# Kernel tuning notes

Measured on AMD Instinct MI355X. Metric: run time of the kernel, lower is better.

## Reference

```python
import jax, jax.numpy as jnp
import numpy as np

V, E, H, HC = 20000, 300, 512, 256
B, N, LE, NW, LW, NC, LC = 16, 64, 16, 8, 16, 64, 16


def _gru_dir(xg, W_hh, b_hh, reverse):
    # xg: [B, T, 3*Hc] precomputed input gates; returns final hidden [B, Hc]
    xs = jnp.swapaxes(xg, 0, 1)
    if reverse:
        xs = xs[::-1]
    h0 = jnp.zeros((xg.shape[0], W_hh.shape[1]), xg.dtype)

    def step(h, xt):
        hr, hz, hn = jnp.split(h @ W_hh.T + b_hh, 3, axis=-1)
        xr, xz, xn = jnp.split(xt, 3, axis=-1)
        r = jax.nn.sigmoid(xr + hr)
        z = jax.nn.sigmoid(xz + hz)
        n = jnp.tanh(xn + r * hn)
        return (1.0 - z) * n + z * h, None

    hT, _ = jax.lax.scan(step, h0, xs)
    return hT


def _bigru(x, Wif, Whf, bif, bhf, Wib, Whb, bib, bhb):
    # x: [B, T, D] -> concat(fwd final, bwd final) = [B, 2*Hc]  (matches torch h_n.permute(1,0,2).reshape)
    hf = _gru_dir(x @ Wif.T + bif, Whf, bhf, False)
    hb = _gru_dir(x @ Wib.T + bib, Whb, bhb, True)
    return jnp.concatenate([hf, hb], axis=-1)


def setup_inputs() -> dict:
    key = jax.random.key(0)
    ks = iter(jax.random.split(key, 64))
    f = lambda *s: jax.random.normal(next(ks), s, jnp.float32) * 0.05
    ri = lambda *s: jax.random.randint(next(ks), s, 0, V)
    return {
        "emb_table": f(V, E),
        "W_prj": f(H, E),
        "dn_Wif": f(3 * HC, H), "dn_Whf": f(3 * HC, HC), "dn_bif": f(3 * HC), "dn_bhf": f(3 * HC),
        "dn_Wib": f(3 * HC, H), "dn_Whb": f(3 * HC, HC), "dn_bib": f(3 * HC), "dn_bhb": f(3 * HC),
        "W_e": f(H, H), "W_l": f(H, H), "W_w": f(H, H),
        "Wg": f(H, H), "bg": f(H),
        "diff_Wif": f(3 * H, H), "diff_Whf": f(3 * H, H), "diff_bif": f(3 * H), "diff_bhf": f(3 * H),
        "diff_Wib": f(3 * H, H), "diff_Whb": f(3 * H, H), "diff_bib": f(3 * H), "diff_bhb": f(3 * H),
        "Wc": f(1, 2 * H), "bc": f(1),
        "Wa1": f(2 * H, 2 * H), "ba1": f(2 * H), "Wa2": f(1, 2 * H), "ba2": f(1),
        "local_adj": jnp.zeros((64, 64), jnp.float32),
        "obs": ri(B, 32),
        "local_graph": ri(64, 8),
        "entities": ri(B, N, LE),
        "locals_": ri(B, N, LE),
        "worlds": ri(B, N, NW, LW),
        "commands": ri(B, NC, LC),
    }


def reference(emb_table, W_prj,
              dn_Wif, dn_Whf, dn_bif, dn_bhf, dn_Wib, dn_Whb, dn_bib, dn_bhb,
              W_e, W_l, W_w, Wg, bg,
              diff_Wif, diff_Whf, diff_bif, diff_bhf, diff_Wib, diff_Whb, diff_bib, diff_bhb,
              Wc, bc, Wa1, ba1, Wa2, ba2,
              local_adj, obs, local_graph, entities, locals_, worlds, commands):
    dn = (dn_Wif, dn_Whf, dn_bif, dn_bhf, dn_Wib, dn_Whb, dn_bib, dn_bhb)
    emb = lambda ids: emb_table[ids] @ W_prj.T  # embedding lookup + no-bias projection to H

    b, n, le = entities.shape
    ent_h = _bigru(emb(entities).reshape(b * n, le, H), *dn).reshape(b, n, H)
    ll = locals_.shape[-1]
    loc_h = _bigru(emb(locals_).reshape(b * n, ll, H), *dn).reshape(b, n, H)
    nw, lw = worlds.shape[2], worlds.shape[3]
    w_h = _bigru(emb(worlds).reshape(b * n * nw, lw, H), *dn).reshape(b, n, nw, H)
    worlds_sum = (w_h @ W_w).sum(axis=2)  # [b, n, H]

    # torch.ones(H,H) + W_e  ==  broadcastable 1.0 + W_e
    graph_hidden = jax.nn.elu(ent_h @ (1.0 + W_e)) + jax.nn.elu(loc_h @ W_l) + worlds_sum
    graph_encoding = jax.nn.elu(jax.nn.elu(graph_hidden) @ Wg.T + bg)  # graph_prj (dropout=eval identity)

    # value network: 'diff' path
    diff_h = _bigru(graph_encoding, diff_Wif, diff_Whf, diff_bif, diff_bhf,
                    diff_Wib, diff_Whb, diff_bib, diff_bhb)  # [b, 2H]
    value = (diff_h @ Wc.T + bc).reshape(b, 1, 1)

    nc, lc = commands.shape[1], commands.shape[2]
    c_h = _bigru(emb(commands).reshape(b * nc, lc, H), *dn).reshape(b, nc, H)

    rep = jnp.concatenate([
        jnp.broadcast_to(c_h[:, None, :, :], (b, n, nc, H)),
        jnp.broadcast_to(graph_encoding[:, :, None, :], (b, n, nc, H)),
    ], axis=-1)  # [b, n, nc, 2H]
    s = jax.nn.elu(rep @ Wa1.T + ba1) @ Wa2.T + ba2  # att_cmd (dropout p=0)
    scores = s[..., 0].mean(axis=1)  # mean over entities -> [b, nc]

    mask = commands.sum(axis=2) > 0
    probs = jax.nn.softmax(jnp.where(mask, scores, -1e9), axis=1)
    index = jnp.argmax(probs, axis=1).reshape(1, b, 1)  # deterministic stand-in for multinomial(1)
    return scores, index, value
```

## Files before the change

kernel.cpp:

```cpp
#include <hip/hip_runtime.h>
#include <stdint.h>

#define DEVFN __device__ __forceinline__

typedef __attribute__((ext_vector_type(4))) float fx4;
typedef __attribute__((ext_vector_type(8))) short sx8;
typedef __bf16 bf16x8 __attribute__((ext_vector_type(8)));

DEVFN float eluf(float x){ return x>0.f ? x : __expf(x)-1.f; }
DEVFN float sigm(float x){ return 1.f/(1.f+__expf(-x)); }
DEVFN float tanhf_(float x){ float cx=fminf(10.f,fmaxf(-10.f,x)); float e=__expf(-2.f*cx); return (1.f-e)/(1.f+e); }

DEVFN fx4 MFMA(sx8 a, sx8 b, fx4 c){
  return __builtin_amdgcn_mfma_f32_16x16x32_bf16(
      __builtin_bit_cast(bf16x8,a), __builtin_bit_cast(bf16x8,b), c, 0,0,0);
}
DEVFN void splitf(float x, short& hi, short& lo){
  __bf16 h = (__bf16)x; hi = __builtin_bit_cast(short, h);
  __bf16 l = (__bf16)(x - (float)h); lo = __builtin_bit_cast(short, l);
}

struct TT { const float* src; float* dst; int srows, scols, drows; };
struct TTs { TT t[4]; };
__global__ void k_prep_t(TTs ts){
  TT tk = ts.t[blockIdx.y];
  size_t tot = (size_t)tk.drows * tk.srows;
  for (size_t i = (size_t)blockIdx.x*256 + threadIdx.x; i < tot; i += (size_t)gridDim.x*256){
    int c = (int)(i / tk.srows), r = (int)(i % tk.srows);
    tk.dst[i] = (c < tk.scols) ? tk.src[(size_t)r*tk.scols + c] : 0.f;
  }
}
struct PL { const float* src; __bf16* hi; __bf16* lo; size_t n; };
struct PLs { PL t[2]; };
__global__ void k_prep_planes(PLs ts){
  PL tk = ts.t[blockIdx.y];
  for (size_t i = (size_t)blockIdx.x*256 + threadIdx.x; i < tk.n; i += (size_t)gridDim.x*256){
    float x = tk.src[i];
    __bf16 h = (__bf16)x;
    tk.hi[i] = h; tk.lo[i] = (__bf16)(x - (float)h);
  }
}
struct BC { const float* src; __bf16* dst; size_t n; };
struct BCs { BC t[2]; };
__global__ void k_prep_b16(BCs ts){
  BC tk = ts.t[blockIdx.y];
  for (size_t i = (size_t)blockIdx.x*256 + threadIdx.x; i < tk.n; i += (size_t)gridDim.x*256)
    tk.dst[i] = (__bf16)tk.src[i];
}

template<int EPI, int OBF>
__global__ __launch_bounds__(256) void gemm_k(
    const float* __restrict__ A, const float* __restrict__ B,
    const float* __restrict__ bias, void* __restrict__ out,
    int M, int N, int Kpad, int Kreal, int lda, int ldb)
{
  int bm = blockIdx.x*64, bn = blockIdx.y*64;
  int tid = threadIdx.x, l = tid&63, w = tid>>6;
  int wm = (w>>1)*32, wn = (w&1)*32;
  int lr = l&15, lk = l>>4;
  fx4 acc[2][2] = {};
  for (int k0 = 0; k0 < Kpad; k0 += 32) {
    sx8 ahi[2], alo[2], bhi[2], blo[2];
    bool full = (k0 + 32 <= Kreal);
    #pragma unroll
    for (int i=0;i<2;i++){
      int row = bm + wm + i*16 + lr; row = row < M ? row : M-1;
      int col = bn + wn + i*16 + lr;
      const float* ap = A + (size_t)row*lda + k0 + lk*8;
      const float* bp = B + (size_t)col*ldb + k0 + lk*8;
      float av[8], bv[8];
      if (full){
        *(fx4*)av = *(const fx4*)ap; *(fx4*)(av+4) = *(const fx4*)(ap+4);
        *(fx4*)bv = *(const fx4*)bp; *(fx4*)(bv+4) = *(const fx4*)(bp+4);
      } else {
        #pragma unroll
        for (int j=0;j<8;j++){
          int k = k0 + lk*8 + j;
          av[j] = (k < Kreal) ? ap[j] : 0.f;
          bv[j] = (k < Kreal) ? bp[j] : 0.f;
        }
      }
      #pragma unroll
      for (int j=0;j<8;j++){
        short h,lo2; splitf(av[j], h, lo2); ahi[i][j]=h; alo[i][j]=lo2;
        splitf(bv[j], h, lo2); bhi[i][j]=h; blo[i][j]=lo2;
      }
    }
    #pragma unroll
    for (int i=0;i<2;i++)
      #pragma unroll
      for (int j=0;j<2;j++){
        acc[i][j] = MFMA(alo[i], bhi[j], acc[i][j]);
        acc[i][j] = MFMA(ahi[i], blo[j], acc[i][j]);
        acc[i][j] = MFMA(ahi[i], bhi[j], acc[i][j]);
      }
  }
  #pragma unroll
  for (int i=0;i<2;i++)
    #pragma unroll
    for (int j=0;j<2;j++)
      #pragma unroll
      for (int q=0;q<4;q++){
        int m = bm + wm + i*16 + lk*4 + q;
        int n = bn + wn + j*16 + lr;
        if (m < M){
          float v = acc[i][j][q];
          if (EPI>=1) v += bias[n];
          if (EPI==2) v = eluf(v);
          if (OBF) ((__bf16*)out)[(size_t)m*N + n] = (__bf16)v;
          else     ((float*)out)[(size_t)m*N + n] = v;
        }
      }
}

__global__ __launch_bounds__(512,2) void dn_gru(
  const float* __restrict__ T,
  const __bf16* __restrict__ Whi, const __bf16* __restrict__ Wlo,
  const float* __restrict__ bh,
  const int* __restrict__ ents, const int* __restrict__ locs,
  const int* __restrict__ wrl, const int* __restrict__ cmd,
  float* __restrict__ seqh, int dir)
{
  __shared__ __align__(16) __bf16 hhi[64*256];
  __shared__ __align__(16) __bf16 hlo[64*256];
  __shared__ int toks[64];
  int wg = blockIdx.x;
  int cb = wg*64;
  int tid = threadIdx.x, l = tid&63, wn = tid>>6;
  int lr = l&15, lk = l>>4;
  float bR[2], bZ[2], bN[2];
  #pragma unroll
  for (int jb=0;jb<2;jb++){
    int j = wn*32 + jb*16 + lr;
    bR[jb]=bh[j]; bZ[jb]=bh[256+j]; bN[jb]=bh[512+j];
  }
  for (int i=tid;i<64*256;i+=512){ hhi[i]=(__bf16)0.f; hlo[i]=(__bf16)0.f; }
  for (int s=0;s<16;s++){
    __syncthreads();
    if (tid<64){
      int c = cb+tid; const int* tp;
      if (c<1024) tp = ents + c*16;
      else if (c<2048) tp = locs + (c-1024)*16;
      else if (c<10240) tp = wrl + (c-2048)*16;
      else tp = cmd + (c-10240)*16;
      toks[tid] = tp[dir? 15-s : s];
    }
    __syncthreads();
    fx4 acc[4][6] = {};
    for (int kk=0;kk<8;kk++){
      sx8 ah[4], al[4];
      #pragma unroll
      for (int mt=0;mt<4;mt++){
        int row = mt*16 + lr;
        int c = (kk*4+lk) ^ (row&31);
        ah[mt] = *(const sx8*)&hhi[row*256 + c*8];
        al[mt] = *(const sx8*)&hlo[row*256 + c*8];
      }
      #pragma unroll
      for (int jb=0;jb<2;jb++)
        #pragma unroll
        for (int role=0;role<3;role++){
          int col = role*256 + wn*32 + jb*16 + lr;
          sx8 bh_ = *(const sx8*)(Whi + (size_t)col*256 + kk*32 + lk*8);
          sx8 bl_ = *(const sx8*)(Wlo + (size_t)col*256 + kk*32 + lk*8);
          #pragma unroll
          for (int mt=0;mt<4;mt++){
            fx4 a = acc[mt][jb*3+role];
            a = MFMA(al[mt], bh_, a);
            a = MFMA(ah[mt], bl_, a);
            a = MFMA(ah[mt], bh_, a);
            acc[mt][jb*3+role] = a;
          }
        }
    }
    float hnew[4][4][2];
    #pragma unroll
    for (int mt=0;mt<4;mt++){
      #pragma unroll
      for (int q=0;q<4;q++){
        int m = mt*16 + lk*4 + q;
        const float* trow = T + (size_t)toks[m]*768;
        #pragma unroll
        for (int jb=0;jb<2;jb++){
          int j = wn*32 + jb*16 + lr;
          float hr = acc[mt][jb*3+0][q] + bR[jb];
          float hz = acc[mt][jb*3+1][q] + bZ[jb];
          float hn = acc[mt][jb*3+2][q] + bN[jb];
          float xr = trow[j], xz = trow[256+j], xn = trow[512+j];
          int cc = ((j>>3) ^ (m&31));
          int hidx = m*256 + cc*8 + (j&7);
          float ho = (float)hhi[hidx] + (float)hlo[hidx];
          float r = sigm(xr+hr), z = sigm(xz+hz);
          float n = tanhf_(xn + r*hn);
          hnew[mt][q][jb] = (1.f-z)*n + z*ho;
        }
      }
    }
    if (s < 15){
      __syncthreads();
      #pragma unroll
      for (int mt=0;mt<4;mt++)
        #pragma unroll
        for (int q=0;q<4;q++)
          #pragma unroll
          for (int jb=0;jb<2;jb++){
            int m = mt*16 + lk*4 + q;
            int j = wn*32 + jb*16 + lr;
            int cc = ((j>>3) ^ (m&31));
            int hidx = m*256 + cc*8 + (j&7);
            float v = hnew[mt][q][jb];
            __bf16 h = (__bf16)v;
            hhi[hidx] = h; hlo[hidx] = (__bf16)(v - (float)h);
          }
    } else {
      #pragma unroll
      for (int mt=0;mt<4;mt++)
        #pragma unroll
        for (int q=0;q<4;q++)
          #pragma unroll
          for (int jb=0;jb<2;jb++){
            int m = mt*16 + lk*4 + q;
            int j = wn*32 + jb*16 + lr;
            seqh[(size_t)(cb+m)*512 + dir*256 + j] = hnew[mt][q][jb];
          }
    }
  }
}

__global__ void k_wsum(const float* __restrict__ seqh, float* __restrict__ ws){
  int r = blockIdx.x;
  for (int c = threadIdx.x; c < 512; c += 256){
    float a = 0.f;
    #pragma unroll
    for (int w8=0; w8<8; w8++) a += seqh[((size_t)2048 + r*8 + w8)*512 + c];
    ws[(size_t)r*512 + c] = a;
  }
}
__global__ void k_rowsum(const float* __restrict__ seqh, float* __restrict__ rs){
  int r = blockIdx.x, l = threadIdx.x;
  float a = 0.f;
  for (int c=l;c<512;c+=64) a += seqh[(size_t)r*512+c];
  #pragma unroll
  for (int o=32;o>0;o>>=1) a += __shfl_down(a,o);
  if (l==0) rs[r]=a;
}
__global__ void k_combine(const float* __restrict__ E1, const float* __restrict__ E2,
                          const float* __restrict__ E3, const float* __restrict__ rs,
                          float* __restrict__ y){
  size_t i = (size_t)blockIdx.x*256 + threadIdx.x;
  int r = (int)(i >> 9);
  float g = eluf(E1[i] + rs[r]) + eluf(E2[i]) + E3[i];
  y[i] = eluf(g);
}

__global__ __launch_bounds__(256) void diff_step(
  const float* __restrict__ hsrc, float* __restrict__ hdst,
  const __bf16* __restrict__ Whf, const __bf16* __restrict__ Whb,
  const float* __restrict__ bhf, const float* __restrict__ bhb,
  const __bf16* __restrict__ Xf, const __bf16* __restrict__ Xb, int t)
{
  int wg = blockIdx.x;
  int dir = wg>>3, seg = wg&7;
  const __bf16* W = dir? Whb: Whf;
  const float* bh = dir? bhb: bhf;
  const __bf16* X = dir? Xb: Xf;
  int tt = dir? 63-t : t;
  int tid = threadIdx.x, l = tid&63, w = tid>>6;
  int lr=l&15, lk=l>>4;
  int jbase = seg*64 + w*16;
  fx4 acc[3] = {};
  const float* hrow = hsrc + (size_t)dir*16*512;
  for (int kk=0;kk<16;kk++){
    const float* ap = hrow + (size_t)lr*512 + kk*32 + lk*8;
    float av[8];
    *(fx4*)av = *(const fx4*)ap; *(fx4*)(av+4) = *(const fx4*)(ap+4);
    sx8 ah, al;
    #pragma unroll
    for (int j=0;j<8;j++){ short h,lo; splitf(av[j],h,lo); ah[j]=h; al[j]=lo; }
    #pragma unroll
    for (int role=0;role<3;role++){
      int col = role*512 + jbase + lr;
      sx8 b = *(const sx8*)(W + (size_t)col*512 + kk*32 + lk*8);
      acc[role] = MFMA(al, b, acc[role]);
      acc[role] = MFMA(ah, b, acc[role]);
    }
  }
  #pragma unroll
  for (int q=0;q<4;q++){
    int m = lk*4+q;
    int j = jbase + lr;
    float hr = acc[0][q] + bh[j];
    float hz = acc[1][q] + bh[512+j];
    float hn = acc[2][q] + bh[1024+j];
    const __bf16* xrow = X + ((size_t)m*64 + tt)*1536;
    float xr = (float)xrow[j], xz = (float)xrow[512+j], xn = (float)xrow[1024+j];
    float ho = hrow[(size_t)m*512 + j];
    float r = sigm(xr+hr), z = sigm(xz+hz);
    float n = tanhf_(xn + r*hn);
    hdst[((size_t)dir*16 + m)*512 + j] = (1.f-z)*n + z*ho;
  }
}

__global__ __launch_bounds__(256) void k_score(
  const float* __restrict__ Amat, const float* __restrict__ Gmat,
  const float* __restrict__ Wa2, const float* __restrict__ ba2, float* __restrict__ sc)
{
  __shared__ float red[4];
  int p = blockIdx.x, b = p>>6, tid = threadIdx.x;
  float av[4], wv[4];
  #pragma unroll
  for (int k=0;k<4;k++){ av[k] = Amat[(size_t)p*1024 + tid + k*256]; wv[k] = Wa2[tid + k*256]; }
  float acc = 0.f;
  for (int n=0;n<64;n++){
    const float* g = Gmat + ((size_t)b*64+n)*1024;
    #pragma unroll
    for (int k=0;k<4;k++) acc += wv[k]*eluf(av[k] + g[tid + k*256]);
  }
  #pragma unroll
  for (int o=32;o>0;o>>=1) acc += __shfl_down(acc,o);
  if ((tid&63)==0) red[tid>>6] = acc;
  __syncthreads();
  if (tid==0) sc[p] = (red[0]+red[1]+red[2]+red[3])*(1.f/64.f) + ba2[0];
}

__global__ void k_final(const float* __restrict__ sc, const int* __restrict__ cmds,
                        const float* __restrict__ hfin, const float* __restrict__ Wc,
                        const float* __restrict__ bc, float* __restrict__ out)
{
  int b = blockIdx.x, l = threadIdx.x;
  out[b*64+l] = sc[b*64+l];
  int ssum = 0;
  const int* cr = cmds + (b*64+l)*16;
  #pragma unroll
  for (int k=0;k<16;k++) ssum += cr[k];
  float v = ssum>0 ? sc[b*64+l] : -1e9f;
  int idx = l;
  #pragma unroll
  for (int o=32;o>0;o>>=1){
    float ov = __shfl_down(v,o); int oi = __shfl_down(idx,o);
    if (ov > v || (ov==v && oi<idx)) { v=ov; idx=oi; }
  }
  if (l==0) out[1024 + b] = (float)idx;
  float a = 0.f;
  for (int j=l;j<512;j+=64) a += hfin[(size_t)b*512+j] * Wc[j];
  for (int j=l;j<512;j+=64) a += hfin[(size_t)(16+b)*512+j] * Wc[512+j];
  #pragma unroll
  for (int o=32;o>0;o>>=1) a += __shfl_down(a,o);
  if (l==0) out[1040 + b] = a + bc[0];
}

static inline void launch_gemm(hipStream_t st, const float* A, const float* B,
                               const float* bias, void* out, int M, int N,
                               int Kpad, int Kreal, int lda, int ldb, int epi, int obf)
{
  dim3 g((M+63)/64, N/64), blk(256);
  if      (epi==0 && obf==0) gemm_k<0,0><<<g,blk,0,st>>>(A,B,bias,out,M,N,Kpad,Kreal,lda,ldb);
  else if (epi==1 && obf==0) gemm_k<1,0><<<g,blk,0,st>>>(A,B,bias,out,M,N,Kpad,Kreal,lda,ldb);
  else if (epi==2 && obf==0) gemm_k<2,0><<<g,blk,0,st>>>(A,B,bias,out,M,N,Kpad,Kreal,lda,ldb);
  else                       gemm_k<1,1><<<g,blk,0,st>>>(A,B,bias,out,M,N,Kpad,Kreal,lda,ldb);
}

extern "C" void kernel_launch(void* const* d_in, const int* in_sizes, int n_in,
                              void* d_out, int out_size, void* d_ws, size_t ws_size,
                              hipStream_t stream) {
  (void)in_sizes; (void)n_in; (void)out_size; (void)ws_size;
  const float* emb   = (const float*)d_in[0];
  const float* W_prj = (const float*)d_in[1];
  const float* dnWif = (const float*)d_in[2];
  const float* dnWhf = (const float*)d_in[3];
  const float* dnbif = (const float*)d_in[4];
  const float* dnbhf = (const float*)d_in[5];
  const float* dnWib = (const float*)d_in[6];
  const float* dnWhb = (const float*)d_in[7];
  const float* dnbib = (const float*)d_in[8];
  const float* dnbhb = (const float*)d_in[9];
  const float* W_e   = (const float*)d_in[10];
  const float* W_l   = (const float*)d_in[11];
  const float* W_w   = (const float*)d_in[12];
  const float* Wg    = (const float*)d_in[13];
  const float* bg    = (const float*)d_in[14];
  const float* dWif  = (const float*)d_in[15];
  const float* dWhf  = (const float*)d_in[16];
  const float* dbif  = (const float*)d_in[17];
  const float* dbhf  = (const float*)d_in[18];
  const float* dWib  = (const float*)d_in[19];
  const float* dWhb  = (const float*)d_in[20];
  const float* dbib  = (const float*)d_in[21];
  const float* dbhb  = (const float*)d_in[22];
  const float* Wc    = (const float*)d_in[23];
  const float* bc    = (const float*)d_in[24];
  const float* Wa1   = (const float*)d_in[25];
  const float* ba1   = (const float*)d_in[26];
  const float* Wa2   = (const float*)d_in[27];
  const float* ba2   = (const float*)d_in[28];
  const int* ents = (const int*)d_in[32];
  const int* locs = (const int*)d_in[33];
  const int* wrl  = (const int*)d_in[34];
  const int* cmds = (const int*)d_in[35];

  char* ws = (char*)d_ws;
  size_t off = 0;
#define WSP(name, type, count) type* name = (type*)(ws + off); off += (((size_t)(count))*sizeof(type) + 255) & ~(size_t)255;
  WSP(pT,     float, 20000*768);
  WSP(pWprjT, float, 320*512);
  WSP(pCf,    float, 768*320);
  WSP(pCb,    float, 768*320);
  WSP(pWhFhi, __bf16, 768*256);
  WSP(pWhFlo, __bf16, 768*256);
  WSP(pWhBhi, __bf16, 768*256);
  WSP(pWhBlo, __bf16, 768*256);
  WSP(pWeT,   float, 512*512);
  WSP(pWlT,   float, 512*512);
  WSP(pWwT,   float, 512*512);
  WSP(pdWhF,  __bf16, 1536*512);
  WSP(pdWhB,  __bf16, 1536*512);
  WSP(pSeqh,  float, 11264*512);
  WSP(pWsum,  float, 1024*512);
  WSP(pRs,    float, 1024);
  WSP(pE1,    float, 1024*512);
  WSP(pE2,    float, 1024*512);
  WSP(pE3,    float, 1024*512);
  WSP(pY,     float, 1024*512);
  WSP(pGe,    float, 1024*512);
  WSP(pXf,    __bf16, 1024*1536);
  WSP(pXb,    __bf16, 1024*1536);
  WSP(pHA,    float, 32*512);
  WSP(pHB,    float, 32*512);
  WSP(pAmat,  float, 1024*1024);
  WSP(pGmat,  float, 1024*1024);
  WSP(pScf,   float, 1024);
#undef WSP

  TTs tt;
  tt.t[0] = { W_prj, pWprjT, 512, 300, 320 };
  tt.t[1] = { W_e,   pWeT,   512, 512, 512 };
  tt.t[2] = { W_l,   pWlT,   512, 512, 512 };
  tt.t[3] = { W_w,   pWwT,   512, 512, 512 };
  k_prep_t<<<dim3(256,4), 256, 0, stream>>>(tt);
  PLs pl;
  pl.t[0] = { dnWhf, pWhFhi, pWhFlo, (size_t)768*256 };
  pl.t[1] = { dnWhb, pWhBhi, pWhBlo, (size_t)768*256 };
  k_prep_planes<<<dim3(256,2), 256, 0, stream>>>(pl);
  BCs bcs;
  bcs.t[0] = { dWhf, pdWhF, (size_t)1536*512 };
  bcs.t[1] = { dWhb, pdWhB, (size_t)1536*512 };
  k_prep_b16<<<dim3(512,2), 256, 0, stream>>>(bcs);

  launch_gemm(stream, dnWif, pWprjT, nullptr, pCf, 768, 320, 512, 512, 512, 512, 0, 0);
  launch_gemm(stream, dnWib, pWprjT, nullptr, pCb, 768, 320, 512, 512, 512, 512, 0, 0);
  launch_gemm(stream, emb, pCf, dnbif, pT, 20000, 768, 320, 300, 300, 320, 1, 0);
  dn_gru<<<176, 512, 0, stream>>>(pT, pWhFhi, pWhFlo, dnbhf, ents, locs, wrl, cmds, pSeqh, 0);
  launch_gemm(stream, emb, pCb, dnbib, pT, 20000, 768, 320, 300, 300, 320, 1, 0);
  dn_gru<<<176, 512, 0, stream>>>(pT, pWhBhi, pWhBlo, dnbhb, ents, locs, wrl, cmds, pSeqh, 1);
  k_wsum<<<1024, 256, 0, stream>>>(pSeqh, pWsum);
  k_rowsum<<<1024, 64, 0, stream>>>(pSeqh, pRs);
  launch_gemm(stream, pSeqh,                   pWeT, nullptr, pE1, 1024, 512, 512, 512, 512, 512, 0, 0);
  launch_gemm(stream, pSeqh + (size_t)1024*512,pWlT, nullptr, pE2, 1024, 512, 512, 512, 512, 512, 0, 0);
  launch_gemm(stream, pWsum,                   pWwT, nullptr, pE3, 1024, 512, 512, 512, 512, 512, 0, 0);
  k_combine<<<2048, 256, 0, stream>>>(pE1, pE2, pE3, pRs, pY);
  launch_gemm(stream, pY, Wg, bg, pGe, 1024, 512, 512, 512, 512, 512, 2, 0);
  launch_gemm(stream, pGe, dWif, dbif, pXf, 1024, 1536, 512, 512, 512, 512, 1, 1);
  launch_gemm(stream, pGe, dWib, dbib, pXb, 1024, 1536, 512, 512, 512, 512, 1, 1);
  launch_gemm(stream, pSeqh + (size_t)10240*512, Wa1, nullptr, pAmat, 1024, 1024, 512, 512, 512, 1024, 0, 0);
  launch_gemm(stream, pGe, Wa1 + 512, ba1, pGmat, 1024, 1024, 512, 512, 512, 1024, 1, 0);
  k_score<<<1024, 256, 0, stream>>>(pAmat, pGmat, Wa2, ba2, pScf);
  hipMemsetAsync(pHA, 0, 32*512*sizeof(float), stream);
  float* ha = pHA; float* hb = pHB;
  for (int t=0; t<64; ++t){
    diff_step<<<16, 256, 0, stream>>>(ha, hb, pdWhF, pdWhB, dbhf, dbhb, pXf, pXb, t);
    float* tmp = ha; ha = hb; hb = tmp;
  }
  k_final<<<16, 64, 0, stream>>>(pScf, cmds, ha, Wc, bc, (float*)d_out);
}
```

Measured before the change: 3.473 ms.

## Fuse diff GRU timesteps into a persistent kernel with grid barrier; halve dn_gru tiles

Replaces 64 per-timestep diff_step launches with one persistent kernel. Its 16 workgroups step through time and synchronise through a global atomic counter barrier, which removes per-step launch overhead. The dn_gru kernel now processes 32 sequences per workgroup instead of 64, doubling the grid to 352 blocks so more CUs are busy, and it uses nontemporal loads and stores for the gate inputs and outputs. The spin barrier relies on all 16 blocks being co-resident, and the final h is still read from pHA, which holds the correct buffer after an even number of swaps.

```diff
diff --git a/kernel.cpp b/kernel.cpp
--- a/kernel.cpp
+++ b/kernel.cpp
@@ -121,11 +121,11 @@
   const int* __restrict__ wrl, const int* __restrict__ cmd,
   float* __restrict__ seqh, int dir)
 {
-  __shared__ __align__(16) __bf16 hhi[64*256];
-  __shared__ __align__(16) __bf16 hlo[64*256];
-  __shared__ int toks[64];
+  __shared__ __align__(16) __bf16 hhi[32*256];
+  __shared__ __align__(16) __bf16 hlo[32*256];
+  __shared__ int toks[32];
   int wg = blockIdx.x;
-  int cb = wg*64;
+  int cb = wg*32;
   int tid = threadIdx.x, l = tid&63, wn = tid>>6;
   int lr = l&15, lk = l>>4;
   float bR[2], bZ[2], bN[2];
@@ -134,10 +134,10 @@
     int j = wn*32 + jb*16 + lr;
     bR[jb]=bh[j]; bZ[jb]=bh[256+j]; bN[jb]=bh[512+j];
   }
-  for (int i=tid;i<64*256;i+=512){ hhi[i]=(__bf16)0.f; hlo[i]=(__bf16)0.f; }
+  for (int i=tid;i<32*256;i+=512){ hhi[i]=(__bf16)0.f; hlo[i]=(__bf16)0.f; }
   for (int s=0;s<16;s++){
     __syncthreads();
-    if (tid<64){
+    if (tid<32){
       int c = cb+tid; const int* tp;
       if (c<1024) tp = ents + c*16;
       else if (c<2048) tp = locs + (c-1024)*16;
@@ -146,11 +146,11 @@
       toks[tid] = tp[dir? 15-s : s];
     }
     __syncthreads();
-    fx4 acc[4][6] = {};
+    fx4 acc[2][6] = {};
     for (int kk=0;kk<8;kk++){
-      sx8 ah[4], al[4];
-      #pragma unroll
-      for (int mt=0;mt<4;mt++){
+      sx8 ah[2], al[2];
+      #pragma unroll
+      for (int mt=0;mt<2;mt++){
         int row = mt*16 + lr;
         int c = (kk*4+lk) ^ (row&31);
         ah[mt] = *(const sx8*)&hhi[row*256 + c*8];
@@ -164,7 +164,7 @@
           sx8 bh_ = *(const sx8*)(Whi + (size_t)col*256 + kk*32 + lk*8);
           sx8 bl_ = *(const sx8*)(Wlo + (size_t)col*256 + kk*32 + lk*8);
           #pragma unroll
-          for (int mt=0;mt<4;mt++){
+          for (int mt=0;mt<2;mt++){
             fx4 a = acc[mt][jb*3+role];
             a = MFMA(al[mt], bh_, a);
             a = MFMA(ah[mt], bl_, a);
@@ -173,9 +173,9 @@
           }
         }
     }
-    float hnew[4][4][2];
-    #pragma unroll
-    for (int mt=0;mt<4;mt++){
+    float hnew[2][4][2];
+    #pragma unroll
+    for (int mt=0;mt<2;mt++){
       #pragma unroll
       for (int q=0;q<4;q++){
         int m = mt*16 + lk*4 + q;
@@ -186,7 +186,9 @@
           float hr = acc[mt][jb*3+0][q] + bR[jb];
           float hz = acc[mt][jb*3+1][q] + bZ[jb];
           float hn = acc[mt][jb*3+2][q] + bN[jb];
-          float xr = trow[j], xz = trow[256+j], xn = trow[512+j];
+          float xr = __builtin_nontemporal_load(trow + j);
+          float xz = __builtin_nontemporal_load(trow + 256 + j);
+          float xn = __builtin_nontemporal_load(trow + 512 + j);
           int cc = ((j>>3) ^ (m&31));
           int hidx = m*256 + cc*8 + (j&7);
           float ho = (float)hhi[hidx] + (float)hlo[hidx];
@@ -199,7 +201,7 @@
     if (s < 15){
       __syncthreads();
       #pragma unroll
-      for (int mt=0;mt<4;mt++)
+      for (int mt=0;mt<2;mt++)
         #pragma unroll
         for (int q=0;q<4;q++)
           #pragma unroll
@@ -214,14 +216,14 @@
           }
     } else {
       #pragma unroll
-      for (int mt=0;mt<4;mt++)
+      for (int mt=0;mt<2;mt++)
         #pragma unroll
         for (int q=0;q<4;q++)
           #pragma unroll
           for (int jb=0;jb<2;jb++){
             int m = mt*16 + lk*4 + q;
             int j = wn*32 + jb*16 + lr;
-            seqh[(size_t)(cb+m)*512 + dir*256 + j] = hnew[mt][q][jb];
+            __builtin_nontemporal_store(hnew[mt][q][jb], &seqh[(size_t)(cb+m)*512 + dir*256 + j]);
           }
     }
   }
@@ -253,51 +255,67 @@
   y[i] = eluf(g);
 }
 
-__global__ __launch_bounds__(256) void diff_step(
-  const float* __restrict__ hsrc, float* __restrict__ hdst,
+__global__ __launch_bounds__(256) void diff_all(
+  float* __restrict__ hA, float* __restrict__ hB,
   const __bf16* __restrict__ Whf, const __bf16* __restrict__ Whb,
   const float* __restrict__ bhf, const float* __restrict__ bhb,
-  const __bf16* __restrict__ Xf, const __bf16* __restrict__ Xb, int t)
+  const __bf16* __restrict__ Xf, const __bf16* __restrict__ Xb,
+  unsigned* __restrict__ bar)
 {
   int wg = blockIdx.x;
   int dir = wg>>3, seg = wg&7;
   const __bf16* W = dir? Whb: Whf;
   const float* bh = dir? bhb: bhf;
   const __bf16* X = dir? Xb: Xf;
-  int tt = dir? 63-t : t;
   int tid = threadIdx.x, l = tid&63, w = tid>>6;
   int lr=l&15, lk=l>>4;
   int jbase = seg*64 + w*16;
-  fx4 acc[3] = {};
-  const float* hrow = hsrc + (size_t)dir*16*512;
-  for (int kk=0;kk<16;kk++){
-    const float* ap = hrow + (size_t)lr*512 + kk*32 + lk*8;
-    float av[8];
-    *(fx4*)av = *(const fx4*)ap; *(fx4*)(av+4) = *(const fx4*)(ap+4);
-    sx8 ah, al;
-    #pragma unroll
-    for (int j=0;j<8;j++){ short h,lo; splitf(av[j],h,lo); ah[j]=h; al[j]=lo; }
-    #pragma unroll
-    for (int role=0;role<3;role++){
-      int col = role*512 + jbase + lr;
-      sx8 b = *(const sx8*)(W + (size_t)col*512 + kk*32 + lk*8);
-      acc[role] = MFMA(al, b, acc[role]);
-      acc[role] = MFMA(ah, b, acc[role]);
-    }
-  }
-  #pragma unroll
-  for (int q=0;q<4;q++){
-    int m = lk*4+q;
-    int j = jbase + lr;
-    float hr = acc[0][q] + bh[j];
-    float hz = acc[1][q] + bh[512+j];
-    float hn = acc[2][q] + bh[1024+j];
-    const __bf16* xrow = X + ((size_t)m*64 + tt)*1536;
-    float xr = (float)xrow[j], xz = (float)xrow[512+j], xn = (float)xrow[1024+j];
-    float ho = hrow[(size_t)m*512 + j];
-    float r = sigm(xr+hr), z = sigm(xz+hz);
-    float n = tanhf_(xn + r*hn);
-    hdst[((size_t)dir*16 + m)*512 + j] = (1.f-z)*n + z*ho;
+  int j = jbase + lr;
+  float bRv = bh[j], bZv = bh[512+j], bNv = bh[1024+j];
+  float* hsrc = hA; float* hdst = hB;
+  for (int t=0; t<64; ++t){
+    int tt = dir? 63-t : t;
+    fx4 acc[3] = {};
+    const float* hrow = hsrc + (size_t)dir*16*512;
+    for (int kk=0;kk<16;kk++){
+      const float* ap = hrow + (size_t)lr*512 + kk*32 + lk*8;
+      float av[8];
+      *(fx4*)av = *(const fx4*)ap; *(fx4*)(av+4) = *(const fx4*)(ap+4);
+      sx8 ah, al;
+      #pragma unroll
+      for (int jj=0;jj<8;jj++){ short h,lo; splitf(av[jj],h,lo); ah[jj]=h; al[jj]=lo; }
+      #pragma unroll
+      for (int role=0;role<3;role++){
+        int col = role*512 + jbase + lr;
+        sx8 b = *(const sx8*)(W + (size_t)col*512 + kk*32 + lk*8);
+        acc[role] = MFMA(al, b, acc[role]);
+        acc[role] = MFMA(ah, b, acc[role]);
+      }
+    }
+    #pragma unroll
+    for (int q=0;q<4;q++){
+      int m = lk*4+q;
+      float hr = acc[0][q] + bRv;
+      float hz = acc[1][q] + bZv;
+      float hn = acc[2][q] + bNv;
+      const __bf16* xrow = X + ((size_t)m*64 + tt)*1536;
+      float xr = (float)xrow[j], xz = (float)xrow[512+j], xn = (float)xrow[1024+j];
+      float ho = hrow[(size_t)m*512 + j];
+      float r = sigm(xr+hr), z = sigm(xz+hz);
+      float n = tanhf_(xn + r*hn);
+      hdst[((size_t)dir*16 + m)*512 + j] = (1.f-z)*n + z*ho;
+    }
+    __threadfence();
+    __syncthreads();
+    if (tid==0){
+      atomicAdd(bar, 1u);
+      unsigned target = 16u*(unsigned)(t+1);
+      while (__hip_atomic_load(bar, __ATOMIC_RELAXED, __HIP_MEMORY_SCOPE_AGENT) < target)
+        __builtin_amdgcn_s_sleep(2);
+    }
+    __syncthreads();
+    __threadfence();
+    float* tmp = hsrc; hsrc = hdst; hdst = tmp;
   }
 }
 
@@ -429,6 +447,7 @@
   WSP(pAmat,  float, 1024*1024);
   WSP(pGmat,  float, 1024*1024);
   WSP(pScf,   float, 1024);
+  WSP(pBar,   unsigned, 64);
 #undef WSP
 
   TTs tt;
@@ -449,9 +468,9 @@
   launch_gemm(stream, dnWif, pWprjT, nullptr, pCf, 768, 320, 512, 512, 512, 512, 0, 0);
   launch_gemm(stream, dnWib, pWprjT, nullptr, pCb, 768, 320, 512, 512, 512, 512, 0, 0);
   launch_gemm(stream, emb, pCf, dnbif, pT, 20000, 768, 320, 300, 300, 320, 1, 0);
-  dn_gru<<<176, 512, 0, stream>>>(pT, pWhFhi, pWhFlo, dnbhf, ents, locs, wrl, cmds, pSeqh, 0);
+  dn_gru<<<352, 512, 0, stream>>>(pT, pWhFhi, pWhFlo, dnbhf, ents, locs, wrl, cmds, pSeqh, 0);
   launch_gemm(stream, emb, pCb, dnbib, pT, 20000, 768, 320, 300, 300, 320, 1, 0);
-  dn_gru<<<176, 512, 0, stream>>>(pT, pWhBhi, pWhBlo, dnbhb, ents, locs, wrl, cmds, pSeqh, 1);
+  dn_gru<<<352, 512, 0, stream>>>(pT, pWhBhi, pWhBlo, dnbhb, ents, locs, wrl, cmds, pSeqh, 1);
   k_wsum<<<1024, 256, 0, stream>>>(pSeqh, pWsum);
   k_rowsum<<<1024, 64, 0, stream>>>(pSeqh, pRs);
   launch_gemm(stream, pSeqh,                   pWeT, nullptr, pE1, 1024, 512, 512, 512, 512, 512, 0, 0);
@@ -465,10 +484,7 @@
   launch_gemm(stream, pGe, Wa1 + 512, ba1, pGmat, 1024, 1024, 512, 512, 512, 1024, 1, 0);
   k_score<<<1024, 256, 0, stream>>>(pAmat, pGmat, Wa2, ba2, pScf);
   hipMemsetAsync(pHA, 0, 32*512*sizeof(float), stream);
-  float* ha = pHA; float* hb = pHB;
-  for (int t=0; t<64; ++t){
-    diff_step<<<16, 256, 0, stream>>>(ha, hb, pdWhF, pdWhB, dbhf, dbhb, pXf, pXb, t);
-    float* tmp = ha; ha = hb; hb = tmp;
-  }
-  k_final<<<16, 64, 0, stream>>>(pScf, cmds, ha, Wc, bc, (float*)d_out);
-}
+  hipMemsetAsync(pBar, 0, 64*sizeof(unsigned), stream);
+  diff_all<<<16, 256, 0, stream>>>(pHA, pHB, pdWhF, pdWhB, dbhf, dbhb, pXf, pXb, pBar);
+  k_final<<<16, 64, 0, stream>>>(pScf, cmds, pHA, Wc, bc, (float*)d_out);
+}
```

Measured after the change: 4.519 ms. 30.1% more time.

## Split persistent GRU kernel into per-timestep launches with global hidden state

Applied to the files above, without the earlier changes.

Replaces the persistent dn_gru kernel (176 blocks, each holding the hidden state of 64 sequences in LDS across all 16 steps) with a per-timestep dn_step kernel launched on a 176x4 grid. The hidden state moves to ping-pong hi/lo bf16 buffers in global memory, and token indices are precomputed by a new k_toks kernel. The aim is more parallelism: four times as many blocks split the gate columns, so the GPU's CUs are better filled. In exchange it adds 32 kernel launches and global-memory round trips for the hidden state each step. Several scratch buffers now alias the pT region to save workspace.

```diff
diff --git a/kernel.cpp b/kernel.cpp
--- a/kernel.cpp
+++ b/kernel.cpp
@@ -46,6 +46,21 @@
   BC tk = ts.t[blockIdx.y];
   for (size_t i = (size_t)blockIdx.x*256 + threadIdx.x; i < tk.n; i += (size_t)gridDim.x*256)
     tk.dst[i] = (__bf16)tk.src[i];
+}
+__global__ void k_toks(const int* __restrict__ ents, const int* __restrict__ locs,
+                       const int* __restrict__ wrl, const int* __restrict__ cmd,
+                       int* __restrict__ toks){
+  int idx = blockIdx.x*256 + threadIdx.x;
+  if (idx >= 2*16*11264) return;
+  int dir = idx / (16*11264);
+  int rem = idx % (16*11264);
+  int s = rem / 11264, c = rem % 11264;
+  const int* tp;
+  if (c<1024) tp = ents + c*16;
+  else if (c<2048) tp = locs + (c-1024)*16;
+  else if (c<10240) tp = wrl + (c-2048)*16;
+  else tp = cmd + (c-10240)*16;
+  toks[idx] = tp[dir ? 15-s : s];
 }
 
 template<int EPI, int OBF>
@@ -113,116 +128,73 @@
       }
 }
 
-__global__ __launch_bounds__(512,2) void dn_gru(
-  const float* __restrict__ T,
+__global__ __launch_bounds__(256) void dn_step(
+  const __bf16* __restrict__ Hshi, const __bf16* __restrict__ Hslo,
+  __bf16* __restrict__ Hdhi, __bf16* __restrict__ Hdlo,
   const __bf16* __restrict__ Whi, const __bf16* __restrict__ Wlo,
-  const float* __restrict__ bh,
-  const int* __restrict__ ents, const int* __restrict__ locs,
-  const int* __restrict__ wrl, const int* __restrict__ cmd,
-  float* __restrict__ seqh, int dir)
-{
-  __shared__ __align__(16) __bf16 hhi[64*256];
-  __shared__ __align__(16) __bf16 hlo[64*256];
-  __shared__ int toks[64];
-  int wg = blockIdx.x;
-  int cb = wg*64;
-  int tid = threadIdx.x, l = tid&63, wn = tid>>6;
+  const float* __restrict__ bias, const float* __restrict__ T,
+  const int* __restrict__ toks,
+  float* __restrict__ seqh, int s, int dir)
+{
+  int bm = blockIdx.x*64;
+  int bj = blockIdx.y*64;
+  int tid = threadIdx.x, l = tid&63, w = tid>>6;
+  int wm = (w>>1)*32, wn = (w&1)*32;
   int lr = l&15, lk = l>>4;
-  float bR[2], bZ[2], bN[2];
-  #pragma unroll
-  for (int jb=0;jb<2;jb++){
-    int j = wn*32 + jb*16 + lr;
-    bR[jb]=bh[j]; bZ[jb]=bh[256+j]; bN[jb]=bh[512+j];
-  }
-  for (int i=tid;i<64*256;i+=512){ hhi[i]=(__bf16)0.f; hlo[i]=(__bf16)0.f; }
-  for (int s=0;s<16;s++){
-    __syncthreads();
-    if (tid<64){
-      int c = cb+tid; const int* tp;
-      if (c<1024) tp = ents + c*16;
-      else if (c<2048) tp = locs + (c-1024)*16;
-      else if (c<10240) tp = wrl + (c-2048)*16;
-      else tp = cmd + (c-10240)*16;
-      toks[tid] = tp[dir? 15-s : s];
-    }
-    __syncthreads();
-    fx4 acc[4][6] = {};
+  fx4 acc[2][2][3] = {};
+  if (s > 0){
     for (int kk=0;kk<8;kk++){
-      sx8 ah[4], al[4];
-      #pragma unroll
-      for (int mt=0;mt<4;mt++){
-        int row = mt*16 + lr;
-        int c = (kk*4+lk) ^ (row&31);
-        ah[mt] = *(const sx8*)&hhi[row*256 + c*8];
-        al[mt] = *(const sx8*)&hlo[row*256 + c*8];
-      }
-      #pragma unroll
-      for (int jb=0;jb<2;jb++)
+      sx8 ah[2], al[2];
+      #pragma unroll
+      for (int i=0;i<2;i++){
+        int m = bm + wm + i*16 + lr;
+        ah[i] = *(const sx8*)(Hshi + (size_t)m*256 + kk*32 + lk*8);
+        al[i] = *(const sx8*)(Hslo + (size_t)m*256 + kk*32 + lk*8);
+      }
+      #pragma unroll
+      for (int jt=0;jt<2;jt++){
         #pragma unroll
         for (int role=0;role<3;role++){
-          int col = role*256 + wn*32 + jb*16 + lr;
-          sx8 bh_ = *(const sx8*)(Whi + (size_t)col*256 + kk*32 + lk*8);
-          sx8 bl_ = *(const sx8*)(Wlo + (size_t)col*256 + kk*32 + lk*8);
+          int col = role*256 + bj + wn + jt*16 + lr;
+          sx8 bhf = *(const sx8*)(Whi + (size_t)col*256 + kk*32 + lk*8);
+          sx8 blf = *(const sx8*)(Wlo + (size_t)col*256 + kk*32 + lk*8);
           #pragma unroll
-          for (int mt=0;mt<4;mt++){
-            fx4 a = acc[mt][jb*3+role];
-            a = MFMA(al[mt], bh_, a);
-            a = MFMA(ah[mt], bl_, a);
-            a = MFMA(ah[mt], bh_, a);
-            acc[mt][jb*3+role] = a;
+          for (int i=0;i<2;i++){
+            fx4 a = acc[i][jt][role];
+            a = MFMA(al[i], bhf, a);
+            a = MFMA(ah[i], blf, a);
+            a = MFMA(ah[i], bhf, a);
+            acc[i][jt][role] = a;
           }
         }
+      }
     }
-    float hnew[4][4][2];
-    #pragma unroll
-    for (int mt=0;mt<4;mt++){
-      #pragma unroll
-      for (int q=0;q<4;q++){
-        int m = mt*16 + lk*4 + q;
-        const float* trow = T + (size_t)toks[m]*768;
-        #pragma unroll
-        for (int jb=0;jb<2;jb++){
-          int j = wn*32 + jb*16 + lr;
-          float hr = acc[mt][jb*3+0][q] + bR[jb];
-          float hz = acc[mt][jb*3+1][q] + bZ[jb];
-          float hn = acc[mt][jb*3+2][q] + bN[jb];
-          float xr = trow[j], xz = trow[256+j], xn = trow[512+j];
-          int cc = ((j>>3) ^ (m&31));
-          int hidx = m*256 + cc*8 + (j&7);
-          float ho = (float)hhi[hidx] + (float)hlo[hidx];
-          float r = sigm(xr+hr), z = sigm(xz+hz);
-          float n = tanhf_(xn + r*hn);
-          hnew[mt][q][jb] = (1.f-z)*n + z*ho;
-        }
-      }
-    }
-    if (s < 15){
-      __syncthreads();
-      #pragma unroll
-      for (int mt=0;mt<4;mt++)
-        #pragma unroll
-        for (int q=0;q<4;q++)
-          #pragma unroll
-          for (int jb=0;jb<2;jb++){
-            int m = mt*16 + lk*4 + q;
-            int j = wn*32 + jb*16 + lr;
-            int cc = ((j>>3) ^ (m&31));
-            int hidx = m*256 + cc*8 + (j&7);
-            float v = hnew[mt][q][jb];
-            __bf16 h = (__bf16)v;
-            hhi[hidx] = h; hlo[hidx] = (__bf16)(v - (float)h);
-          }
-    } else {
-      #pragma unroll
-      for (int mt=0;mt<4;mt++)
-        #pragma unroll
-        for (int q=0;q<4;q++)
-          #pragma unroll
-          for (int jb=0;jb<2;jb++){
-            int m = mt*16 + lk*4 + q;
-            int j = wn*32 + jb*16 + lr;
-            seqh[(size_t)(cb+m)*512 + dir*256 + j] = hnew[mt][q][jb];
-          }
+  }
+  const int* tks = toks + s*11264;
+  #pragma unroll
+  for (int i=0;i<2;i++){
+    #pragma unroll
+    for (int q=0;q<4;q++){
+      int m = bm + wm + i*16 + lk*4 + q;
+      int tok = tks[m];
+      const float* trow = T + (size_t)tok*768;
+      #pragma unroll
+      for (int jt=0;jt<2;jt++){
+        int j = bj + wn + jt*16 + lr;
+        float hr = acc[i][jt][0][q] + bias[j];
+        float hz = acc[i][jt][1][q] + bias[256+j];
+        float hn = acc[i][jt][2][q] + bias[512+j];
+        float xr = trow[j], xz = trow[256+j], xn = trow[512+j];
+        float ho = 0.f;
+        if (s > 0) ho = (float)Hshi[(size_t)m*256+j] + (float)Hslo[(size_t)m*256+j];
+        float r = sigm(xr+hr), z = sigm(xz+hz);
+        float n = tanhf_(xn + r*hn);
+        float v = (1.f-z)*n + z*ho;
+        __bf16 hh = (__bf16)v;
+        Hdhi[(size_t)m*256+j] = hh;
+        Hdlo[(size_t)m*256+j] = (__bf16)(v - (float)hh);
+        if (s == 15) seqh[(size_t)m*512 + dir*256 + j] = v;
+      }
     }
   }
 }
@@ -415,21 +387,28 @@
   WSP(pdWhF,  __bf16, 1536*512);
   WSP(pdWhB,  __bf16, 1536*512);
   WSP(pSeqh,  float, 11264*512);
-  WSP(pWsum,  float, 1024*512);
-  WSP(pRs,    float, 1024);
-  WSP(pE1,    float, 1024*512);
-  WSP(pE2,    float, 1024*512);
-  WSP(pE3,    float, 1024*512);
-  WSP(pY,     float, 1024*512);
-  WSP(pGe,    float, 1024*512);
-  WSP(pXf,    __bf16, 1024*1536);
-  WSP(pXb,    __bf16, 1024*1536);
+  WSP(pH0hi,  __bf16, 11264*256);
+  WSP(pH0lo,  __bf16, 11264*256);
+  WSP(pH1hi,  __bf16, 11264*256);
+  WSP(pH1lo,  __bf16, 11264*256);
+  WSP(pToks,  int,    2*16*11264);
   WSP(pHA,    float, 32*512);
   WSP(pHB,    float, 32*512);
-  WSP(pAmat,  float, 1024*1024);
-  WSP(pGmat,  float, 1024*1024);
+  WSP(pRs,    float, 1024);
   WSP(pScf,   float, 1024);
 #undef WSP
+  const size_t SZ = (size_t)1024*512*4;
+  char* sc = (char*)pT;
+  float* pWsum = (float*)(sc + 0*SZ);
+  float* pE1   = (float*)(sc + 1*SZ);
+  float* pE2   = (float*)(sc + 2*SZ);
+  float* pE3   = (float*)(sc + 3*SZ);
+  float* pY    = (float*)(sc + 4*SZ);
+  float* pGe   = (float*)(sc + 5*SZ);
+  float* pAmat = (float*)(sc + 6*SZ);
+  float* pGmat = (float*)(sc + 8*SZ);
+  __bf16* pXf  = (__bf16*)(sc + 10*SZ);
+  __bf16* pXb  = (__bf16*)(sc + 10*SZ + (size_t)1024*1536*2);
 
   TTs tt;
   tt.t[0] = { W_prj, pWprjT, 512, 300, 320 };
@@ -445,13 +424,27 @@
   bcs.t[0] = { dWhf, pdWhF, (size_t)1536*512 };
   bcs.t[1] = { dWhb, pdWhB, (size_t)1536*512 };
   k_prep_b16<<<dim3(512,2), 256, 0, stream>>>(bcs);
+  k_toks<<<1408, 256, 0, stream>>>(ents, locs, wrl, cmds, pToks);
 
   launch_gemm(stream, dnWif, pWprjT, nullptr, pCf, 768, 320, 512, 512, 512, 512, 0, 0);
   launch_gemm(stream, dnWib, pWprjT, nullptr, pCb, 768, 320, 512, 512, 512, 512, 0, 0);
-  launch_gemm(stream, emb, pCf, dnbif, pT, 20000, 768, 320, 300, 300, 320, 1, 0);
-  dn_gru<<<176, 512, 0, stream>>>(pT, pWhFhi, pWhFlo, dnbhf, ents, locs, wrl, cmds, pSeqh, 0);
-  launch_gemm(stream, emb, pCb, dnbib, pT, 20000, 768, 320, 300, 300, 320, 1, 0);
-  dn_gru<<<176, 512, 0, stream>>>(pT, pWhBhi, pWhBlo, dnbhb, ents, locs, wrl, cmds, pSeqh, 1);
+
+  for (int dir = 0; dir < 2; ++dir){
+    launch_gemm(stream, emb, dir? pCb : pCf, dir? dnbib : dnbif, pT,
+                20000, 768, 320, 300, 300, 320, 1, 0);
+    const __bf16* Whi = dir? pWhBhi : pWhFhi;
+    const __bf16* Wlo = dir? pWhBlo : pWhFlo;
+    const float*  bh  = dir? dnbhb  : dnbhf;
+    const int*    tks = pToks + (size_t)dir*16*11264;
+    for (int s = 0; s < 16; ++s){
+      __bf16 *shi, *slo, *dhi, *dlo;
+      if ((s & 1) == 0){ shi=pH0hi; slo=pH0lo; dhi=pH1hi; dlo=pH1lo; }
+      else             { shi=pH1hi; slo=pH1lo; dhi=pH0hi; dlo=pH0lo; }
+      dn_step<<<dim3(176,4), 256, 0, stream>>>(shi, slo, dhi, dlo,
+          Whi, Wlo, bh, pT, tks, pSeqh, s, dir);
+    }
+  }
+
   k_wsum<<<1024, 256, 0, stream>>>(pSeqh, pWsum);
   k_rowsum<<<1024, 64, 0, stream>>>(pSeqh, pRs);
   launch_gemm(stream, pSeqh,                   pWeT, nullptr, pE1, 1024, 512, 512, 512, 512, 512, 0, 0);
```

Result: faster. 2.859 ms (-17.7%).
